# Kernel optimization log

Hardware: AMD Instinct MI355X
Metric: run time of the kernel (lower is better)

## Reference

```python
import jax, jax.numpy as jnp
import numpy as np

T_START = 0.0
T_END = 1.0
STEPS = 10
HID = 1024
BATCH = 8192


def setup_inputs() -> dict:
    key = jax.random.key(0)
    ks = jax.random.split(key, 7)
    s1 = 1.0 / np.sqrt(HID + 1)
    s2 = 1.0 / np.sqrt(HID)
    return {
        "h": jax.random.normal(ks[0], (BATCH, HID), dtype=jnp.float32),
        "W1": jax.random.uniform(ks[1], (HID + 1, HID), jnp.float32, -s1, s1),
        "b1": jax.random.uniform(ks[2], (HID,), jnp.float32, -s1, s1),
        "W2": jax.random.uniform(ks[3], (HID, HID), jnp.float32, -s2, s2),
        "b2": jax.random.uniform(ks[4], (HID,), jnp.float32, -s2, s2),
        "W3": jax.random.uniform(ks[5], (HID, HID), jnp.float32, -s2, s2),
        "b3": jax.random.uniform(ks[6], (HID,), jnp.float32, -s2, s2),
    }


def reference(h, W1, b1, W2, b2, W3, b3):
    dt = (T_END - T_START) / STEPS

    def dynamics(t, h):
        # concat(h, t*ones) @ W1 == h @ W1[:-1] + t * W1[-1]; keep explicit concat for clarity
        t_vec = jnp.full((h.shape[0], 1), t, dtype=h.dtype)
        x = jnp.concatenate([h, t_vec], axis=1)
        x = jnp.tanh(x @ W1 + b1)
        x = jnp.tanh(x @ W2 + b2)
        return x @ W3 + b3

    def rk4_step(h, t):
        k1 = dynamics(t, h)
        k2 = dynamics(t + dt / 2, h + dt / 2 * k1)
        k3 = dynamics(t + dt / 2, h + dt / 2 * k2)
        k4 = dynamics(t + dt, h + dt * k3)
        return h + dt / 6 * (k1 + 2 * k2 + 2 * k3 + k4), None

    ts = T_START + dt * jnp.arange(STEPS, dtype=h.dtype)
    h_final, _ = jax.lax.scan(rk4_step, h, ts)
    return h_final
```

## Files before the change

kernel.cpp:

```cpp
#include <hip/hip_runtime.h>


typedef __attribute__((ext_vector_type(8))) __bf16 bf16x8;
typedef __attribute__((ext_vector_type(4))) float f32x4;
typedef __attribute__((ext_vector_type(8))) float f32x8;
typedef __attribute__((ext_vector_type(16))) float f32x16;
typedef __attribute__((ext_vector_type(8))) unsigned short us8;
typedef __attribute__((ext_vector_type(4))) int i32x4;
typedef __attribute__((ext_vector_type(8))) int i32x8;
typedef unsigned short ushort_t;
typedef unsigned char u8;

#define SCALE_ONE  0x7F7F7F7Fu
#define SCALE_INV32 0x7A7A7A7Au
#define HW1_SCALE 16.f
#define HW1_INV   0.0625f

#define GLOAD16(gp, lp) \
  __builtin_amdgcn_global_load_lds((const __attribute__((address_space(1))) unsigned int*)(gp), \
                                   (__attribute__((address_space(3))) unsigned int*)(lp), 16, 0, 0)

__device__ __forceinline__ ushort_t f2bf(float f) {
  union { float f; unsigned u; } v; v.f = f;
  unsigned r = v.u + 0x7fffu + ((v.u >> 16) & 1u);
  return (ushort_t)(r >> 16);
}
__device__ __forceinline__ float b2f(ushort_t u) {
  union { unsigned u; float f; } v; v.u = ((unsigned)u) << 16; return v.f;
}
__device__ __forceinline__ float fast_tanh(float x) {
  float e = __expf(2.0f * x);
  return 1.0f - 2.0f * __builtin_amdgcn_rcpf(e + 1.0f);
}
__device__ __forceinline__ uint2 pack_fp8x8(const float* v) {
  int a = __builtin_amdgcn_cvt_pk_fp8_f32(v[0], v[1], 0, false);
  a = __builtin_amdgcn_cvt_pk_fp8_f32(v[2], v[3], a, true);
  int b = __builtin_amdgcn_cvt_pk_fp8_f32(v[4], v[5], 0, false);
  b = __builtin_amdgcn_cvt_pk_fp8_f32(v[6], v[7], b, true);
  return make_uint2((unsigned)a, (unsigned)b);
}
__device__ __forceinline__ void fp8x4_to_f32(unsigned q, float* o) {
  o[0] = __builtin_amdgcn_cvt_f32_fp8(q, 0);
  o[1] = __builtin_amdgcn_cvt_f32_fp8(q, 1);
  o[2] = __builtin_amdgcn_cvt_f32_fp8(q, 2);
  o[3] = __builtin_amdgcn_cvt_f32_fp8(q, 3);
}
__device__ __forceinline__ void fp8x8_to_f32(uint2 q, float* o) {
  fp8x4_to_f32(q.x, o); fp8x4_to_f32(q.y, o + 4);
}

__global__ void transpose_bf16(const float* __restrict__ in, ushort_t* __restrict__ out) {
  __shared__ float tile[32][33];
  const int bx = blockIdx.x * 32, by = blockIdx.y * 32;
  const int tx = threadIdx.x, ty = threadIdx.y;
#pragma unroll
  for (int i = 0; i < 32; i += 8)
    tile[ty + i][tx] = in[(size_t)(by + ty + i) * 1024 + bx + tx];
  __syncthreads();
#pragma unroll
  for (int i = 0; i < 32; i += 8)
    out[(size_t)(bx + ty + i) * 1024 + by + tx] = f2bf(tile[tx][ty + i]);
}

__global__ void transpose_fp8(const float* __restrict__ in, u8* __restrict__ out) {
  __shared__ float tile[32][33];
  const int bx = blockIdx.x * 32, by = blockIdx.y * 32;
  const int tx = threadIdx.x, ty = threadIdx.y;
#pragma unroll
  for (int i = 0; i < 32; i += 8)
    tile[ty + i][tx] = in[(size_t)(by + ty + i) * 1024 + bx + tx];
  __syncthreads();
#pragma unroll
  for (int i = 0; i < 32; i += 8) {
    const float v = 32.f * tile[tx][ty + i];
    int r = __builtin_amdgcn_cvt_pk_fp8_f32(v, v, 0, false);
    out[(size_t)(bx + ty + i) * 1024 + by + tx] = (u8)(r & 0xFF);
  }
}

__global__ void conv_bf16(const float* __restrict__ in, ushort_t* __restrict__ out) {
  size_t i = ((size_t)blockIdx.x * 256 + threadIdx.x) * 4;
  float4 v = *(const float4*)&in[i];
  ushort4 o;
  o.x = f2bf(v.x); o.y = f2bf(v.y); o.z = f2bf(v.z); o.w = f2bf(v.w);
  *(ushort4*)&out[i] = o;
}

__global__ void c31_kernel(const ushort_t* __restrict__ W1t, const float* __restrict__ b3,
                           float* __restrict__ c31) {
  const int j = blockIdx.x * 256 + threadIdx.x;
  float acc = 0.f;
  for (int c = 0; c < 128; ++c) {
    const us8 w = *(const us8*)&W1t[(size_t)j * 1024 + c * 8];
    const f32x8 b = *(const f32x8*)&b3[c * 8];
#pragma unroll
    for (int e = 0; e < 8; ++e) acc += b2f(w[e]) * b[e];
  }
  c31[j] = acc;
}

__global__ void xtfold(const u8* __restrict__ a, const u8* __restrict__ b,
                       const u8* __restrict__ c, const u8* __restrict__ d,
                       ushort_t* __restrict__ XT) {
  const size_t i = ((size_t)blockIdx.x * 256 + threadIdx.x) * 8;
  float va[8], vb[8], vc[8], vd[8];
  fp8x8_to_f32(*(const uint2*)&a[i], va);
  fp8x8_to_f32(*(const uint2*)&b[i], vb);
  fp8x8_to_f32(*(const uint2*)&c[i], vc);
  fp8x8_to_f32(*(const uint2*)&d[i], vd);
  const us8 xo = *(const us8*)&XT[i];
  us8 xn;
#pragma unroll
  for (int e = 0; e < 8; ++e)
    xn[e] = f2bf(b2f(xo[e]) + va[e] + 2.f * (vb[e] + vc[e]) + vd[e]);
  *(us8*)&XT[i] = xn;
}

template<int MODE>
__global__ void __launch_bounds__(256, 2)
gemm_bf16(const ushort_t* __restrict__ Ag, const ushort_t* __restrict__ Bg,
          const float* __restrict__ bias,
          u8* __restrict__ out8b, u8* __restrict__ out8,
          const float* __restrict__ h0f, float* __restrict__ outf)
{
  constexpr int K = 1024, NCOL = 1024, NT = 16;
  constexpr float DT = 0.1f;
  __shared__ __align__(16) ushort_t lds[2][16384];

  const int bid = blockIdx.x;
  const int nb = (int)gridDim.x >> 3;
  const int logical = (bid & 7) * nb + (bid >> 3);
  const int bm0 = (logical >> 3) * 128;
  const int bn0 = (logical & 7) * 128;

  const int tid = threadIdx.x;
  const int w = tid >> 6, l = tid & 63;
  const int wr = w >> 1, wc = w & 1;

  const int srow = l >> 3;
  const int sclog = (l & 7) ^ srow;
  const size_t gA0 = (size_t)(bm0 + w * 32 + srow) * K + sclog * 8;
  const size_t gB0 = (size_t)(bn0 + w * 32 + srow) * K + sclog * 8;
  const int ldsAo = w * 2048 + l * 8;
  const int ldsBo = 8192 + w * 2048 + l * 8;

#define STAGEB(s, t1) do { \
    const ushort_t* ga = Ag + gA0 + (size_t)(t1) * 64; \
    const ushort_t* gb = Bg + gB0 + (size_t)(t1) * 64; \
    GLOAD16(ga,          &lds[s][ldsAo]); \
    GLOAD16(ga + 8 * K,  &lds[s][ldsAo + 512]); \
    GLOAD16(ga + 16 * K, &lds[s][ldsAo + 1024]); \
    GLOAD16(ga + 24 * K, &lds[s][ldsAo + 1536]); \
    GLOAD16(gb,          &lds[s][ldsBo]); \
    GLOAD16(gb + 8 * K,  &lds[s][ldsBo + 512]); \
    GLOAD16(gb + 16 * K, &lds[s][ldsBo + 1024]); \
    GLOAD16(gb + 24 * K, &lds[s][ldsBo + 1536]); } while (0)

  const int r = l & 15, kb = l >> 4, xr = r & 7;
  const int aRow = (wr * 64 + r) * 64;
  const int bRow = 8192 + (wc * 64 + r) * 64;
  const int c0 = ((0 | kb) ^ xr) * 8;
  const int c1 = ((4 | kb) ^ xr) * 8;

  f32x4 acc[4][4];
#pragma unroll
  for (int m = 0; m < 4; ++m)
#pragma unroll
    for (int n = 0; n < 4; ++n) acc[m][n] = (f32x4){0.f, 0.f, 0.f, 0.f};

  STAGEB(0, 0);

  for (int t = 0; t < NT; ++t) {
    const int cur = t & 1;
    __builtin_amdgcn_s_barrier();
    if (t + 1 < NT) {
      STAGEB(cur ^ 1, t + 1);
      asm volatile("s_waitcnt vmcnt(8)" ::: "memory");
    } else {
      asm volatile("s_waitcnt vmcnt(0)" ::: "memory");
    }
    __builtin_amdgcn_s_barrier();
    __builtin_amdgcn_sched_barrier(0);

    const ushort_t* Lb = &lds[cur][0];
    bf16x8 av[4], bv[4];
#pragma unroll
    for (int m = 0; m < 4; ++m) av[m] = *(const bf16x8*)(Lb + aRow + m * 1024 + c0);
#pragma unroll
    for (int n = 0; n < 4; ++n) bv[n] = *(const bf16x8*)(Lb + bRow + n * 1024 + c0);
    __builtin_amdgcn_s_setprio(1);
#pragma unroll
    for (int m = 0; m < 4; ++m)
#pragma unroll
      for (int n = 0; n < 4; ++n)
        acc[m][n] = __builtin_amdgcn_mfma_f32_16x16x32_bf16(av[m], bv[n], acc[m][n], 0, 0, 0);
    __builtin_amdgcn_s_setprio(0);
#pragma unroll
    for (int m = 0; m < 4; ++m) av[m] = *(const bf16x8*)(Lb + aRow + m * 1024 + c1);
#pragma unroll
    for (int n = 0; n < 4; ++n) bv[n] = *(const bf16x8*)(Lb + bRow + n * 1024 + c1);
    __builtin_amdgcn_s_setprio(1);
#pragma unroll
    for (int m = 0; m < 4; ++m)
#pragma unroll
      for (int n = 0; n < 4; ++n)
        acc[m][n] = __builtin_amdgcn_mfma_f32_16x16x32_bf16(av[m], bv[n], acc[m][n], 0, 0, 0);
    __builtin_amdgcn_s_setprio(0);
  }
#undef STAGEB

  __syncthreads();
  ushort_t* C = &lds[0][0];
  const int er = (l >> 4) * 4;
  const int ec = l & 15;
#pragma unroll
  for (int n = 0; n < 4; ++n) {
    const int lc = wc * 64 + n * 16 + ec;
#pragma unroll
    for (int m = 0; m < 4; ++m) {
#pragma unroll
      for (int j = 0; j < 4; ++j) {
        const int lr = wr * 64 + m * 16 + er + j;
        C[lr * 136 + lc] = f2bf(acc[m][n][j]);
      }
    }
  }
  __syncthreads();

  constexpr float DT6 = DT / 6.f;
#pragma unroll
  for (int i = 0; i < 8; ++i) {
    const int chunk = tid + i * 256;
    const int row = chunk >> 4;
    const int cc = chunk & 15;
    const int col0 = bn0 + cc * 8;
    const us8 kv8 = *(const us8*)&C[row * 136 + cc * 8];
    const size_t gidx = (size_t)(bm0 + row) * NCOL + col0;

    if (MODE == 0) {
      float v[8];
#pragma unroll
      for (int e = 0; e < 8; ++e) v[e] = 32.f * b2f(kv8[e]);
      *(uint2*)&out8[gidx] = pack_fp8x8(v);
    } else if (MODE == 1) {
      const f32x8 b = *(const f32x8*)&bias[col0];
      float v[8], hv[8];
#pragma unroll
      for (int e = 0; e < 8; ++e) {
        const float c = b2f(kv8[e]);
        hv[e] = HW1_SCALE * c;
        v[e] = fast_tanh(c + b[e]);
      }
      *(uint2*)&out8b[gidx] = pack_fp8x8(hv);
      *(uint2*)&out8[gidx]  = pack_fp8x8(v);
    } else {
      const f32x8 b = *(const f32x8*)&bias[col0];
      const f32x8 h8 = *(const f32x8*)&h0f[gidx];
      f32x8 o;
#pragma unroll
      for (int e = 0; e < 8; ++e) o[e] = h8[e] + DT6 * b2f(kv8[e]) + b[e];
      *(f32x8*)&outf[gidx] = o;
    }
  }
}

template<int MODE>
__global__ void __launch_bounds__(256, 2)
gemm_fp8(const u8* __restrict__ Ag, const u8* __restrict__ Bg,
         const float* __restrict__ bias, const float* __restrict__ wl,
         const float* __restrict__ c31,
         const u8* __restrict__ hW1r,
         const u8* __restrict__ g0p, const u8* __restrict__ g1p, const u8* __restrict__ g2p,
         const u8* __restrict__ x2a, const u8* __restrict__ x2b, const u8* __restrict__ x2c,
         u8* __restrict__ out8, u8* __restrict__ gout,
         ushort_t* __restrict__ bfio, u8* __restrict__ hW1w,
         float p1, float p2, int flag)
{
  constexpr int NT = 8;
  constexpr float DT = 0.1f, DT6 = DT / 6.f;
  __shared__ __align__(16) u8 bufs[2][32768];

  const int bid = blockIdx.x;
  const int nb = (int)gridDim.x >> 3;
  const int logical = (bid & 7) * nb + (bid >> 3);
  const int bm0 = (logical >> 3) * 128;
  const int bn0 = (logical & 7) * 128;

  const int tid = threadIdx.x;
  const int w = tid >> 6, l = tid & 63;
  const int wr = w >> 1, wc = w & 1;
  const int l31 = l & 31, kg = l >> 5;

  int so[4], ldo[4];
#pragma unroll
  for (int i = 0; i < 4; ++i) {
    const int slot = tid + i * 256;
    const int row = slot >> 3, phys = slot & 7;
    so[i] = row * 1024 + ((phys ^ (row & 7)) << 4);
    ldo[i] = slot << 4;
  }
  const u8* gA = Ag + (size_t)bm0 * 1024;
  const u8* gB = Bg + (size_t)bn0 * 1024;

#define STAGEF(s, t1) do { \
    GLOAD16(gA + so[0] + (t1) * 128, &bufs[s][ldo[0]]); \
    GLOAD16(gA + so[1] + (t1) * 128, &bufs[s][ldo[1]]); \
    GLOAD16(gA + so[2] + (t1) * 128, &bufs[s][ldo[2]]); \
    GLOAD16(gA + so[3] + (t1) * 128, &bufs[s][ldo[3]]); \
    GLOAD16(gB + so[0] + (t1) * 128, &bufs[s][16384 + ldo[0]]); \
    GLOAD16(gB + so[1] + (t1) * 128, &bufs[s][16384 + ldo[1]]); \
    GLOAD16(gB + so[2] + (t1) * 128, &bufs[s][16384 + ldo[2]]); \
    GLOAD16(gB + so[3] + (t1) * 128, &bufs[s][16384 + ldo[3]]); } while (0)

  auto ldsAddr = [](int row, int c) -> int {
    return row * 128 + ((c ^ (row & 7)) << 4);
  };
  const int ra0 = wr * 64 + l31, ra1 = ra0 + 32;
  const int rb0 = wc * 64 + l31, rb1 = rb0 + 32;
  const int ck0 = kg * 2, ck1 = 4 + kg * 2;
  const int a00 = ldsAddr(ra0, ck0), a00b = ldsAddr(ra0, ck0 + 1);
  const int a10 = ldsAddr(ra1, ck0), a10b = ldsAddr(ra1, ck0 + 1);
  const int b00 = 16384 + ldsAddr(rb0, ck0), b00b = 16384 + ldsAddr(rb0, ck0 + 1);
  const int b10 = 16384 + ldsAddr(rb1, ck0), b10b = 16384 + ldsAddr(rb1, ck0 + 1);
  const int a01 = ldsAddr(ra0, ck1), a01b = ldsAddr(ra0, ck1 + 1);
  const int a11 = ldsAddr(ra1, ck1), a11b = ldsAddr(ra1, ck1 + 1);
  const int b01 = 16384 + ldsAddr(rb0, ck1), b01b = 16384 + ldsAddr(rb0, ck1 + 1);
  const int b11 = 16384 + ldsAddr(rb1, ck1), b11b = 16384 + ldsAddr(rb1, ck1 + 1);

  f32x16 acc00, acc01, acc10, acc11;
#pragma unroll
  for (int i = 0; i < 16; ++i) { acc00[i] = 0.f; acc01[i] = 0.f; acc10[i] = 0.f; acc11[i] = 0.f; }

#define LD8(dst, o0, o1) do { \
    i32x4 lo_ = *(const i32x4*)(Lb + (o0)); \
    i32x4 hi_ = *(const i32x4*)(Lb + (o1)); \
    dst = (i32x8){lo_[0], lo_[1], lo_[2], lo_[3], hi_[0], hi_[1], hi_[2], hi_[3]}; } while (0)

  STAGEF(0, 0);

  for (int t = 0; t < NT; ++t) {
    const int cur = t & 1;
    __builtin_amdgcn_s_barrier();
    if (t + 1 < NT) {
      STAGEF(cur ^ 1, t + 1);
      asm volatile("s_waitcnt vmcnt(8)" ::: "memory");
    } else {
      asm volatile("s_waitcnt vmcnt(0)" ::: "memory");
    }
    __builtin_amdgcn_s_barrier();
    __builtin_amdgcn_sched_barrier(0);

    const u8* Lb = &bufs[cur][0];
    i32x8 a0, a1, b0, b1;
    LD8(a0, a00, a00b);
    LD8(a1, a10, a10b);
    LD8(b0, b00, b00b);
    LD8(b1, b10, b10b);
    __builtin_amdgcn_s_setprio(1);
    acc00 = __builtin_amdgcn_mfma_scale_f32_32x32x64_f8f6f4(a0, b0, acc00, 0, 0, 0, SCALE_ONE, 0, SCALE_INV32);
    acc01 = __builtin_amdgcn_mfma_scale_f32_32x32x64_f8f6f4(a0, b1, acc01, 0, 0, 0, SCALE_ONE, 0, SCALE_INV32);
    acc10 = __builtin_amdgcn_mfma_scale_f32_32x32x64_f8f6f4(a1, b0, acc10, 0, 0, 0, SCALE_ONE, 0, SCALE_INV32);
    acc11 = __builtin_amdgcn_mfma_scale_f32_32x32x64_f8f6f4(a1, b1, acc11, 0, 0, 0, SCALE_ONE, 0, SCALE_INV32);
    __builtin_amdgcn_s_setprio(0);
    LD8(a0, a01, a01b);
    LD8(a1, a11, a11b);
    LD8(b0, b01, b01b);
    LD8(b1, b11, b11b);
    __builtin_amdgcn_s_setprio(1);
    acc00 = __builtin_amdgcn_mfma_scale_f32_32x32x64_f8f6f4(a0, b0, acc00, 0, 0, 0, SCALE_ONE, 0, SCALE_INV32);
    acc01 = __builtin_amdgcn_mfma_scale_f32_32x32x64_f8f6f4(a0, b1, acc01, 0, 0, 0, SCALE_ONE, 0, SCALE_INV32);
    acc10 = __builtin_amdgcn_mfma_scale_f32_32x32x64_f8f6f4(a1, b0, acc10, 0, 0, 0, SCALE_ONE, 0, SCALE_INV32);
    acc11 = __builtin_amdgcn_mfma_scale_f32_32x32x64_f8f6f4(a1, b1, acc11, 0, 0, 0, SCALE_ONE, 0, SCALE_INV32);
    __builtin_amdgcn_s_setprio(0);
  }
#undef STAGEF

  uint2 hw_pre[8];
  if (MODE == 3 || MODE == 4) {
#pragma unroll
    for (int i = 0; i < 8; ++i) {
      const int chunk = tid + i * 256;
      const size_t gidx = (size_t)(bm0 + (chunk >> 4)) * 1024 + bn0 + (chunk & 15) * 8;
      hw_pre[i] = *(const uint2*)&hW1r[gidx];
    }
  }
  uint2 g0_pre[8], g1_pre[8], g2_pre[8];
  if (MODE == 4) {
#pragma unroll
    for (int i = 0; i < 8; ++i) {
      const int chunk = tid + i * 256;
      const size_t gidx = (size_t)(bm0 + (chunk >> 4)) * 1024 + bn0 + (chunk & 15) * 8;
      g0_pre[i] = *(const uint2*)&g0p[gidx];
      g1_pre[i] = *(const uint2*)&g1p[gidx];
      g2_pre[i] = *(const uint2*)&g2p[gidx];
    }
  }

  __syncthreads();
  ushort_t* Cst = (ushort_t*)&bufs[0][0];
#define STORE_ACC(A_, mm, nn) do { \
    _Pragma("unroll") \
    for (int reg = 0; reg < 16; ++reg) { \
      const int lrow = wr * 64 + (mm) * 32 + (reg & 3) + 8 * (reg >> 2) + 4 * kg; \
      const int lcol = wc * 64 + (nn) * 32 + l31; \
      Cst[lrow * 136 + lcol] = f2bf(A_[reg]); } } while (0)
  STORE_ACC(acc00, 0, 0);
  STORE_ACC(acc01, 0, 1);
  STORE_ACC(acc10, 1, 0);
  STORE_ACC(acc11, 1, 1);
#undef STORE_ACC
  __syncthreads();

#pragma unroll
  for (int i = 0; i < 8; ++i) {
    const int chunk = tid + i * 256;
    const int row = chunk >> 4;
    const int cc = chunk & 15;
    const int col0 = bn0 + cc * 8;
    const us8 kv8 = *(const us8*)&Cst[row * 136 + cc * 8];
    const size_t gidx = (size_t)(bm0 + row) * 1024 + col0;

    if (MODE == 2) {
      const f32x8 b = *(const f32x8*)&bias[col0];
      float x2v[8];
#pragma unroll
      for (int e = 0; e < 8; ++e) x2v[e] = fast_tanh(b2f(kv8[e]) + b[e]);
      *(uint2*)&out8[gidx] = pack_fp8x8(x2v);
    } else if (MODE == 3) {
      const f32x8 b  = *(const f32x8*)&bias[col0];
      const f32x8 wv = *(const f32x8*)&wl[col0];
      const f32x8 cv = *(const f32x8*)&c31[col0];
      float hwv[8];
      fp8x8_to_f32(hw_pre[i], hwv);
      float gv[8], x1v[8];
#pragma unroll
      for (int e = 0; e < 8; ++e) {
        gv[e] = b2f(kv8[e]);
        x1v[e] = fast_tanh(hwv[e] * HW1_INV + p1 * (gv[e] + cv[e]) + b[e] + p2 * wv[e]);
      }
      *(uint2*)&gout[gidx] = pack_fp8x8(gv);
      *(uint2*)&out8[gidx] = pack_fp8x8(x1v);
    } else {
      const f32x8 b  = *(const f32x8*)&bias[col0];
      const f32x8 wv = *(const f32x8*)&wl[col0];
      const f32x8 cv = *(const f32x8*)&c31[col0];
      float hwv[8];
      fp8x8_to_f32(hw_pre[i], hwv);
      float g0v[8], g1v[8], g2v[8];
      fp8x8_to_f32(g0_pre[i], g0v);
      fp8x8_to_f32(g1_pre[i], g1v);
      fp8x8_to_f32(g2_pre[i], g2v);
      float va[8], vb[8], vc[8], vd[8];
      fp8x8_to_f32(*(const uint2*)&x2a[gidx], va);
      fp8x8_to_f32(*(const uint2*)&x2b[gidx], vb);
      fp8x8_to_f32(*(const uint2*)&x2c[gidx], vc);
      fp8x8_to_f32(*(const uint2*)&Ag[gidx], vd);
      us8 xtn;
      if (flag) {
#pragma unroll
        for (int e = 0; e < 8; ++e)
          xtn[e] = f2bf(va[e] + 2.f * (vb[e] + vc[e]) + vd[e]);
      } else {
        const us8 xo = *(const us8*)&bfio[gidx];
#pragma unroll
        for (int e = 0; e < 8; ++e)
          xtn[e] = f2bf(b2f(xo[e]) + va[e] + 2.f * (vb[e] + vc[e]) + vd[e]);
      }
      *(us8*)&bfio[gidx] = xtn;
      float x1v[8], hn16[8];
#pragma unroll
      for (int e = 0; e < 8; ++e) {
        const float gs = g0v[e] + 2.f * (g1v[e] + g2v[e]) + b2f(kv8[e]);
        const float hn = hwv[e] * HW1_INV + DT6 * gs + DT * cv[e];
        hn16[e] = HW1_SCALE * hn;
        x1v[e] = fast_tanh(hn + b[e] + p2 * wv[e]);
      }
      *(uint2*)&hW1w[gidx] = pack_fp8x8(hn16);
      *(uint2*)&out8[gidx] = pack_fp8x8(x1v);
    }
  }
}

extern "C" void kernel_launch(void* const* d_in, const int* in_sizes, int n_in,
                              void* d_out, int out_size, void* d_ws, size_t ws_size,
                              hipStream_t stream) {
  (void)in_sizes; (void)n_in; (void)out_size; (void)ws_size;
  const float* h_in = (const float*)d_in[0];
  const float* W1   = (const float*)d_in[1];
  const float* b1   = (const float*)d_in[2];
  const float* b2   = (const float*)d_in[4];
  const float* W2   = (const float*)d_in[3];
  const float* W3   = (const float*)d_in[5];
  const float* b3   = (const float*)d_in[6];
  const float* W1last = W1 + (size_t)1024 * 1024;

  char* ws = (char*)d_ws;
  ushort_t* W1t   = (ushort_t*)(ws);
  u8*       W2t8  = (u8*)      (ws + (2ull << 20));
  u8*       Bt318 = (u8*)      (ws + (3ull << 20));
  float*    c31   = (float*)   (ws + (4ull << 20));
  u8*       hW18  = (u8*)      (ws + (8ull << 20));
  u8*       x1    = (u8*)      (ws + (24ull << 20));
  u8*       x2s0  = (u8*)      (ws + (32ull << 20));
  u8*       x2s1  = (u8*)      (ws + (40ull << 20));
  u8*       x2s2  = (u8*)      (ws + (48ull << 20));
  u8*       x2s3  = (u8*)      (ws + (56ull << 20));
  ushort_t* XT    = (ushort_t*)(ws + (64ull << 20));
  u8*       g0    = (u8*)d_out;
  u8*       g1    = (u8*)d_out + (8ull << 20);
  u8*       g2    = (u8*)d_out + (16ull << 20);
  ushort_t* hb    = (ushort_t*)d_out;
  float*    OUT   = (float*)d_out;

  const float dt = 0.1f;
  constexpr int GRID = 512, BLK = 256;
  dim3 tb(32, 8), tg(32, 32);

  transpose_bf16<<<tg, tb, 0, stream>>>(W1, W1t);
  transpose_fp8 <<<tg, tb, 0, stream>>>(W2, W2t8);
  conv_bf16<<<1024, 256, 0, stream>>>(W3, XT);
  conv_bf16<<<8192, 256, 0, stream>>>(h_in, hb);
  c31_kernel<<<4, 256, 0, stream>>>(W1t, b3, c31);
  gemm_bf16<0><<<64, BLK, 0, stream>>>(W1t, XT, nullptr, nullptr, Bt318, nullptr, nullptr);
  gemm_bf16<1><<<GRID, BLK, 0, stream>>>(hb, W1t, b1, hW18, x1, nullptr, nullptr);

  for (int step = 0; step < 10; ++step) {
    const float t0 = step * dt;
    gemm_fp8<2><<<GRID, BLK, 0, stream>>>(x1, W2t8, b2, nullptr, nullptr, nullptr,
                                          nullptr, nullptr, nullptr, nullptr, nullptr, nullptr,
                                          x2s0, nullptr, nullptr, nullptr, 0.f, 0.f, 0);
    gemm_fp8<3><<<GRID, BLK, 0, stream>>>(x2s0, Bt318, b1, W1last, c31, hW18,
                                          nullptr, nullptr, nullptr, nullptr, nullptr, nullptr,
                                          x1, g0, nullptr, nullptr, 0.5f * dt, t0 + 0.5f * dt, 0);
    gemm_fp8<2><<<GRID, BLK, 0, stream>>>(x1, W2t8, b2, nullptr, nullptr, nullptr,
                                          nullptr, nullptr, nullptr, nullptr, nullptr, nullptr,
                                          x2s1, nullptr, nullptr, nullptr, 0.f, 0.f, 0);
    gemm_fp8<3><<<GRID, BLK, 0, stream>>>(x2s1, Bt318, b1, W1last, c31, hW18,
                                          nullptr, nullptr, nullptr, nullptr, nullptr, nullptr,
                                          x1, g1, nullptr, nullptr, 0.5f * dt, t0 + 0.5f * dt, 0);
    gemm_fp8<2><<<GRID, BLK, 0, stream>>>(x1, W2t8, b2, nullptr, nullptr, nullptr,
                                          nullptr, nullptr, nullptr, nullptr, nullptr, nullptr,
                                          x2s2, nullptr, nullptr, nullptr, 0.f, 0.f, 0);
    gemm_fp8<3><<<GRID, BLK, 0, stream>>>(x2s2, Bt318, b1, W1last, c31, hW18,
                                          nullptr, nullptr, nullptr, nullptr, nullptr, nullptr,
                                          x1, g2, nullptr, nullptr, dt, t0 + dt, 0);
    gemm_fp8<2><<<GRID, BLK, 0, stream>>>(x1, W2t8, b2, nullptr, nullptr, nullptr,
                                          nullptr, nullptr, nullptr, nullptr, nullptr, nullptr,
                                          x2s3, nullptr, nullptr, nullptr, 0.f, 0.f, 0);
    if (step < 9) {
      gemm_fp8<4><<<GRID, BLK, 0, stream>>>(x2s3, Bt318, b1, W1last, c31, hW18,
                                            g0, g1, g2, x2s0, x2s1, x2s2,
                                            x1, nullptr, XT, hW18,
                                            0.f, t0 + dt, (step == 0));
    }
  }
  xtfold<<<4096, 256, 0, stream>>>(x2s0, x2s1, x2s2, x2s3, XT);

  transpose_bf16<<<tg, tb, 0, stream>>>(W3, W1t);
  gemm_bf16<5><<<GRID, BLK, 0, stream>>>(XT, W1t, b3, nullptr, nullptr, h_in, OUT);
}
```

Measured before the change: 1.429 ms.

## Halve FP8 GEMM K-tile to shrink LDS and double occupancy

The fp8 GEMM's per-stage K tile drops from 128 to 64 bytes, so the double-buffered LDS shrinks from 64KB to about 35KB, and launch bounds rise from 2 to 4 blocks per CU. The LDS swizzle and global source offsets are rebuilt for the narrower tile, with two rows packed per 128-byte LDS line, and the loop runs 16 iterations with one MFMA group each. The epilogue prefetch of hW1/g buffers now happens after the accumulator stores, which lowers register pressure during the main loop. In exchange there are twice as many barriers per K step and less latency hiding per stage, and register pressure must fit the tighter launch bound.

```diff
diff --git a/kernel.cpp b/kernel.cpp
--- a/kernel.cpp
+++ b/kernel.cpp
@@ -265,7 +265,7 @@
 }
 
 template<int MODE>
-__global__ void __launch_bounds__(256, 2)
+__global__ void __launch_bounds__(256, 4)
 gemm_fp8(const u8* __restrict__ Ag, const u8* __restrict__ Bg,
          const float* __restrict__ bias, const float* __restrict__ wl,
          const float* __restrict__ c31,
@@ -276,9 +276,9 @@
          ushort_t* __restrict__ bfio, u8* __restrict__ hW1w,
          float p1, float p2, int flag)
 {
-  constexpr int NT = 8;
+  constexpr int NT = 16;
   constexpr float DT = 0.1f, DT6 = DT / 6.f;
-  __shared__ __align__(16) u8 bufs[2][32768];
+  __shared__ __align__(16) u8 ldsraw[35840];
 
   const int bid = blockIdx.x;
   const int nb = (int)gridDim.x >> 3;
@@ -291,41 +291,33 @@
   const int wr = w >> 1, wc = w & 1;
   const int l31 = l & 31, kg = l >> 5;
 
-  int so[4], ldo[4];
-#pragma unroll
-  for (int i = 0; i < 4; ++i) {
-    const int slot = tid + i * 256;
-    const int row = slot >> 3, phys = slot & 7;
-    so[i] = row * 1024 + ((phys ^ (row & 7)) << 4);
-    ldo[i] = slot << 4;
-  }
+  auto srcoff = [](int slot) -> int {
+    int rp = slot >> 3, p = slot & 7, q = p ^ (rp & 7);
+    return (2 * rp + (q >> 2)) * 1024 + (q & 3) * 16;
+  };
+  const int so0 = srcoff(tid), so1 = srcoff(256 + tid);
   const u8* gA = Ag + (size_t)bm0 * 1024;
   const u8* gB = Bg + (size_t)bn0 * 1024;
+  const int ld0 = tid * 16, ld1 = 4096 + tid * 16;
 
 #define STAGEF(s, t1) do { \
-    GLOAD16(gA + so[0] + (t1) * 128, &bufs[s][ldo[0]]); \
-    GLOAD16(gA + so[1] + (t1) * 128, &bufs[s][ldo[1]]); \
-    GLOAD16(gA + so[2] + (t1) * 128, &bufs[s][ldo[2]]); \
-    GLOAD16(gA + so[3] + (t1) * 128, &bufs[s][ldo[3]]); \
-    GLOAD16(gB + so[0] + (t1) * 128, &bufs[s][16384 + ldo[0]]); \
-    GLOAD16(gB + so[1] + (t1) * 128, &bufs[s][16384 + ldo[1]]); \
-    GLOAD16(gB + so[2] + (t1) * 128, &bufs[s][16384 + ldo[2]]); \
-    GLOAD16(gB + so[3] + (t1) * 128, &bufs[s][16384 + ldo[3]]); } while (0)
-
-  auto ldsAddr = [](int row, int c) -> int {
-    return row * 128 + ((c ^ (row & 7)) << 4);
+    u8* base = ldsraw + (s) * 16384; \
+    GLOAD16(gA + so0 + (t1) * 64, base + ld0); \
+    GLOAD16(gA + so1 + (t1) * 64, base + ld1); \
+    GLOAD16(gB + so0 + (t1) * 64, base + 8192 + ld0); \
+    GLOAD16(gB + so1 + (t1) * 64, base + 8192 + ld1); } while (0)
+
+  auto ldsAddr = [](int r2, int kc) -> int {
+    int q = ((r2 & 1) << 2) | kc; int p = q ^ ((r2 >> 1) & 7);
+    return (r2 >> 1) * 128 + p * 16;
   };
+  const int kc2 = kg * 2;
   const int ra0 = wr * 64 + l31, ra1 = ra0 + 32;
   const int rb0 = wc * 64 + l31, rb1 = rb0 + 32;
-  const int ck0 = kg * 2, ck1 = 4 + kg * 2;
-  const int a00 = ldsAddr(ra0, ck0), a00b = ldsAddr(ra0, ck0 + 1);
-  const int a10 = ldsAddr(ra1, ck0), a10b = ldsAddr(ra1, ck0 + 1);
-  const int b00 = 16384 + ldsAddr(rb0, ck0), b00b = 16384 + ldsAddr(rb0, ck0 + 1);
-  const int b10 = 16384 + ldsAddr(rb1, ck0), b10b = 16384 + ldsAddr(rb1, ck0 + 1);
-  const int a01 = ldsAddr(ra0, ck1), a01b = ldsAddr(ra0, ck1 + 1);
-  const int a11 = ldsAddr(ra1, ck1), a11b = ldsAddr(ra1, ck1 + 1);
-  const int b01 = 16384 + ldsAddr(rb0, ck1), b01b = 16384 + ldsAddr(rb0, ck1 + 1);
-  const int b11 = 16384 + ldsAddr(rb1, ck1), b11b = 16384 + ldsAddr(rb1, ck1 + 1);
+  const int aA00 = ldsAddr(ra0, kc2), aA01 = ldsAddr(ra0, kc2 + 1);
+  const int aA10 = ldsAddr(ra1, kc2), aA11 = ldsAddr(ra1, kc2 + 1);
+  const int bA00 = 8192 + ldsAddr(rb0, kc2), bA01 = 8192 + ldsAddr(rb0, kc2 + 1);
+  const int bA10 = 8192 + ldsAddr(rb1, kc2), bA11 = 8192 + ldsAddr(rb1, kc2 + 1);
 
   f32x16 acc00, acc01, acc10, acc11;
 #pragma unroll
@@ -343,61 +335,30 @@
     __builtin_amdgcn_s_barrier();
     if (t + 1 < NT) {
       STAGEF(cur ^ 1, t + 1);
-      asm volatile("s_waitcnt vmcnt(8)" ::: "memory");
+      asm volatile("s_waitcnt vmcnt(4)" ::: "memory");
     } else {
       asm volatile("s_waitcnt vmcnt(0)" ::: "memory");
     }
     __builtin_amdgcn_s_barrier();
     __builtin_amdgcn_sched_barrier(0);
 
-    const u8* Lb = &bufs[cur][0];
+    const u8* Lb = ldsraw + cur * 16384;
     i32x8 a0, a1, b0, b1;
-    LD8(a0, a00, a00b);
-    LD8(a1, a10, a10b);
-    LD8(b0, b00, b00b);
-    LD8(b1, b10, b10b);
+    LD8(a0, aA00, aA01);
+    LD8(a1, aA10, aA11);
+    LD8(b0, bA00, bA01);
+    LD8(b1, bA10, bA11);
     __builtin_amdgcn_s_setprio(1);
     acc00 = __builtin_amdgcn_mfma_scale_f32_32x32x64_f8f6f4(a0, b0, acc00, 0, 0, 0, SCALE_ONE, 0, SCALE_INV32);
     acc01 = __builtin_amdgcn_mfma_scale_f32_32x32x64_f8f6f4(a0, b1, acc01, 0, 0, 0, SCALE_ONE, 0, SCALE_INV32);
     acc10 = __builtin_amdgcn_mfma_scale_f32_32x32x64_f8f6f4(a1, b0, acc10, 0, 0, 0, SCALE_ONE, 0, SCALE_INV32);
     acc11 = __builtin_amdgcn_mfma_scale_f32_32x32x64_f8f6f4(a1, b1, acc11, 0, 0, 0, SCALE_ONE, 0, SCALE_INV32);
     __builtin_amdgcn_s_setprio(0);
-    LD8(a0, a01, a01b);
-    LD8(a1, a11, a11b);
-    LD8(b0, b01, b01b);
-    LD8(b1, b11, b11b);
-    __builtin_amdgcn_s_setprio(1);
-    acc00 = __builtin_amdgcn_mfma_scale_f32_32x32x64_f8f6f4(a0, b0, acc00, 0, 0, 0, SCALE_ONE, 0, SCALE_INV32);
-    acc01 = __builtin_amdgcn_mfma_scale_f32_32x32x64_f8f6f4(a0, b1, acc01, 0, 0, 0, SCALE_ONE, 0, SCALE_INV32);
-    acc10 = __builtin_amdgcn_mfma_scale_f32_32x32x64_f8f6f4(a1, b0, acc10, 0, 0, 0, SCALE_ONE, 0, SCALE_INV32);
-    acc11 = __builtin_amdgcn_mfma_scale_f32_32x32x64_f8f6f4(a1, b1, acc11, 0, 0, 0, SCALE_ONE, 0, SCALE_INV32);
-    __builtin_amdgcn_s_setprio(0);
   }
 #undef STAGEF
 
-  uint2 hw_pre[8];
-  if (MODE == 3 || MODE == 4) {
-#pragma unroll
-    for (int i = 0; i < 8; ++i) {
-      const int chunk = tid + i * 256;
-      const size_t gidx = (size_t)(bm0 + (chunk >> 4)) * 1024 + bn0 + (chunk & 15) * 8;
-      hw_pre[i] = *(const uint2*)&hW1r[gidx];
-    }
-  }
-  uint2 g0_pre[8], g1_pre[8], g2_pre[8];
-  if (MODE == 4) {
-#pragma unroll
-    for (int i = 0; i < 8; ++i) {
-      const int chunk = tid + i * 256;
-      const size_t gidx = (size_t)(bm0 + (chunk >> 4)) * 1024 + bn0 + (chunk & 15) * 8;
-      g0_pre[i] = *(const uint2*)&g0p[gidx];
-      g1_pre[i] = *(const uint2*)&g1p[gidx];
-      g2_pre[i] = *(const uint2*)&g2p[gidx];
-    }
-  }
-
   __syncthreads();
-  ushort_t* Cst = (ushort_t*)&bufs[0][0];
+  ushort_t* Cst = (ushort_t*)&ldsraw[0];
 #define STORE_ACC(A_, mm, nn) do { \
     _Pragma("unroll") \
     for (int reg = 0; reg < 16; ++reg) { \
@@ -409,6 +370,27 @@
   STORE_ACC(acc10, 1, 0);
   STORE_ACC(acc11, 1, 1);
 #undef STORE_ACC
+
+  uint2 hw_pre[8];
+  if (MODE == 3 || MODE == 4) {
+#pragma unroll
+    for (int i = 0; i < 8; ++i) {
+      const int chunk = tid + i * 256;
+      const size_t gidx = (size_t)(bm0 + (chunk >> 4)) * 1024 + bn0 + (chunk & 15) * 8;
+      hw_pre[i] = *(const uint2*)&hW1r[gidx];
+    }
+  }
+  uint2 g0_pre[8], g1_pre[8], g2_pre[8];
+  if (MODE == 4) {
+#pragma unroll
+    for (int i = 0; i < 8; ++i) {
+      const int chunk = tid + i * 256;
+      const size_t gidx = (size_t)(bm0 + (chunk >> 4)) * 1024 + bn0 + (chunk & 15) * 8;
+      g0_pre[i] = *(const uint2*)&g0p[gidx];
+      g1_pre[i] = *(const uint2*)&g1p[gidx];
+      g2_pre[i] = *(const uint2*)&g2p[gidx];
+    }
+  }
   __syncthreads();
 
 #pragma unroll
@@ -488,8 +470,8 @@
   const float* h_in = (const float*)d_in[0];
   const float* W1   = (const float*)d_in[1];
   const float* b1   = (const float*)d_in[2];
+  const float* W2   = (const float*)d_in[3];
   const float* b2   = (const float*)d_in[4];
-  const float* W2   = (const float*)d_in[3];
   const float* W3   = (const float*)d_in[5];
   const float* b3   = (const float*)d_in[6];
   const float* W1last = W1 + (size_t)1024 * 1024;
```

Measured after the change: 1.559 ms. +9.1%, slower.
